# Optimization experiments

Measured on AMD Instinct MI355X. Metric: run time of the kernel, lower is better.

## Reference

```python
import jax, jax.numpy as jnp
import numpy as np

T, B, IN = 1000, 16, 440
H0, H1 = 512, 512


def setup_inputs() -> dict:
    key = jax.random.key(0)
    ks = iter(jax.random.split(key, 64))

    def w(shape, s=0.02):
        return jax.random.normal(next(ks), shape, jnp.float32) * s

    inp = {"x": jax.random.normal(next(ks), (T, B, IN), jnp.float32)}
    # layer 0 consumes IN features; layer 1 consumes 2*H0 (bidir concat)
    for li, (din, h) in enumerate([(IN, H0), (2 * H0, H1)]):
        for g in "fioc":
            inp[f"W{g}{li}"] = w((h, din))          # x-gate Linear weight
            inp[f"b{g}{li}"] = jnp.zeros((h,), jnp.float32)  # x-gate bias
            inp[f"U{g}{li}"] = w((h, h))            # recurrent Linear (no bias)
    return inp


def _lstm_layer(x, Wf, bf, Wi, bi, Wo, bo, Wc, bc, Uf, Ui, Uo, Uc):
    # Precompute input-to-gate projections for all timesteps (as the torch code does).
    gf = jnp.einsum('tbi,hi->tbh', x, Wf) + bf
    gi = jnp.einsum('tbi,hi->tbh', x, Wi) + bi
    go = jnp.einsum('tbi,hi->tbh', x, Wo) + bo
    gc = jnp.einsum('tbi,hi->tbh', x, Wc) + bc
    B2, H = x.shape[1], Wf.shape[0]

    def step(carry, g):
        ht, ct = carry
        gft, git, got, gct = g
        ft = jax.nn.sigmoid(gft + ht @ Uf.T)
        it = jax.nn.sigmoid(git + ht @ Ui.T)
        ot = jax.nn.sigmoid(got + ht @ Uo.T)
        # drop_mask == 1.0 in eval mode (lstm_drop = 0.0)
        ct = it * jnp.tanh(gct + ht @ Uc.T) + ft * ct
        ht = ot * jnp.tanh(ct)
        return (ht, ct), ht

    init = (jnp.zeros((B2, H), x.dtype), jnp.zeros((B2, H), x.dtype))
    _, h = jax.lax.scan(step, init, (gf, gi, go, gc))
    return h  # [T, B2, H]


def _bidir_layer(x, params):
    Bb = x.shape[1]
    # bidir: concat forward stream with time-flipped stream along batch dim
    x2 = jnp.concatenate([x, x[::-1]], axis=1)
    h = _lstm_layer(x2, *params)
    h_f = h[:, :Bb]
    h_b = h[:, Bb:][::-1]  # flip backward stream back to forward time
    return jnp.concatenate([h_f, h_b], axis=2)


def reference(x,
              Wf0, bf0, Uf0, Wi0, bi0, Ui0, Wo0, bo0, Uo0, Wc0, bc0, Uc0,
              Wf1, bf1, Uf1, Wi1, bi1, Ui1, Wo1, bo1, Uo1, Wc1, bc1, Uc1):
    p0 = (Wf0, bf0, Wi0, bi0, Wo0, bo0, Wc0, bc0, Uf0, Ui0, Uo0, Uc0)
    p1 = (Wf1, bf1, Wi1, bi1, Wo1, bo1, Wc1, bc1, Uf1, Ui1, Uo1, Uc1)
    h = _bidir_layer(x, p0)
    h = _bidir_layer(h, p1)
    return h  # [T, B, 2*H1]
```

## Files before the change

### kernel.cpp

```cpp
#include <hip/hip_runtime.h>
#include <hip/hip_bf16.h>
#include <stdint.h>


typedef __attribute__((ext_vector_type(8))) short bf16x8;
typedef __attribute__((ext_vector_type(4))) float f32x4;
typedef __attribute__((ext_vector_type(4))) int i32x4;

__device__ __forceinline__ unsigned short f2bf(float f) {
    union { float f; unsigned int u; } v; v.f = f;
    unsigned int u = v.u;
    return (unsigned short)((u + 0x7fffu + ((u >> 16) & 1u)) >> 16);
}
__device__ __forceinline__ float bf2f(unsigned short b) {
    union { unsigned int u; float f; } v; v.u = ((unsigned int)b) << 16;
    return v.f;
}
__device__ __forceinline__ float fsig(float x) { return 1.f / (1.f + __expf(-x)); }
__device__ __forceinline__ float ftanh(float x) { return 1.f - 2.f / (1.f + __expf(2.f * x)); }


__device__ __forceinline__ unsigned int coh_ld32(const void* p) {
    unsigned int v;
    asm volatile("global_load_dword %0, %1, off sc0 sc1\n\ts_waitcnt vmcnt(0)"
                 : "=v"(v) : "v"(p) : "memory");
    return v;
}
__device__ __forceinline__ void coh_ld128_issue(i32x4& d, const void* p) {
    asm volatile("global_load_dwordx4 %0, %1, off sc0 sc1" : "=&v"(d) : "v"(p) : "memory");
}
__device__ __forceinline__ void coh_st32(void* p, unsigned int v) {
    asm volatile("global_store_dword %0, %1, off sc0 sc1" :: "v"(p), "v"(v) : "memory");
}
__device__ __forceinline__ void vm_drain() {
    asm volatile("s_waitcnt vmcnt(0)" ::: "memory");
}


__global__ void pack_x_kernel(const float* __restrict__ x, unsigned short* __restrict__ xp,
                              int M, int K, int Kp) {
    int total = M * Kp;
    for (int idx = blockIdx.x * blockDim.x + threadIdx.x; idx < total;
         idx += gridDim.x * blockDim.x) {
        int r = idx / Kp, k = idx - r * Kp;
        xp[idx] = (k < K) ? f2bf(x[(size_t)r * K + k]) : (unsigned short)0;
    }
}

__global__ void pack_w_kernel(const float* __restrict__ Wf, const float* __restrict__ Wi,
                              const float* __restrict__ Wo, const float* __restrict__ Wc,
                              unsigned short* __restrict__ out, int K, int Kp) {
    int total = 2048 * Kp;
    for (int idx = blockIdx.x * blockDim.x + threadIdx.x; idx < total;
         idx += gridDim.x * blockDim.x) {
        int n = idx / Kp, k = idx - n * Kp;
        int gate = n >> 9, j = n & 511;
        const float* W = (gate == 0) ? Wf : (gate == 1) ? Wi : (gate == 2) ? Wo : Wc;
        out[idx] = (k < K) ? f2bf(W[(size_t)j * K + k]) : (unsigned short)0;
    }
}


__global__ __launch_bounds__(256) void gemm_gates(
    const unsigned short* __restrict__ A, const unsigned short* __restrict__ Bm,
    const float* __restrict__ bF, const float* __restrict__ bI,
    const float* __restrict__ bO, const float* __restrict__ bC,
    unsigned short* __restrict__ G, int Kp) {
    __shared__ unsigned short Alds[64][32];
    __shared__ unsigned short Blds[64][32];
    const int tid = threadIdx.x;
    const int m0 = blockIdx.x * 64;
    const int n0 = blockIdx.y * 64;
    const int w = tid >> 6, l = tid & 63;
    const int lr = l & 15, lk = (l >> 4) * 8;
    const int ldrow = tid >> 2;
    const int ldk = (tid & 3) * 8;
    const unsigned short* Aptr = A + (size_t)(m0 + ldrow) * Kp + ldk;
    const unsigned short* Bptr = Bm + (size_t)(n0 + ldrow) * Kp + ldk;

    f32x4 zero = {0.f, 0.f, 0.f, 0.f};
    f32x4 acc0 = zero, acc1 = zero, acc2 = zero, acc3 = zero;

    for (int k0 = 0; k0 < Kp; k0 += 32) {
        *(uint4*)&Alds[ldrow][ldk] = *(const uint4*)(Aptr + k0);
        *(uint4*)&Blds[ldrow][ldk] = *(const uint4*)(Bptr + k0);
        __syncthreads();
        bf16x8 a = *(const bf16x8*)&Alds[w * 16 + lr][lk];
        bf16x8 b0 = *(const bf16x8*)&Blds[0 * 16 + lr][lk];
        bf16x8 b1 = *(const bf16x8*)&Blds[1 * 16 + lr][lk];
        bf16x8 b2 = *(const bf16x8*)&Blds[2 * 16 + lr][lk];
        bf16x8 b3 = *(const bf16x8*)&Blds[3 * 16 + lr][lk];
        acc0 = __builtin_amdgcn_mfma_f32_16x16x32_bf16(a, b0, acc0, 0, 0, 0);
        acc1 = __builtin_amdgcn_mfma_f32_16x16x32_bf16(a, b1, acc1, 0, 0, 0);
        acc2 = __builtin_amdgcn_mfma_f32_16x16x32_bf16(a, b2, acc2, 0, 0, 0);
        acc3 = __builtin_amdgcn_mfma_f32_16x16x32_bf16(a, b3, acc3, 0, 0, 0);
        __syncthreads();
    }
    const int gate = n0 >> 9;
    const float* bias = (gate == 0) ? bF : (gate == 1) ? bI : (gate == 2) ? bO : bC;
    f32x4 accs[4] = {acc0, acc1, acc2, acc3};
#pragma unroll
    for (int c = 0; c < 4; ++c) {
        int col = n0 + c * 16 + lr;
        float bv = bias[col & 511];
#pragma unroll
        for (int r = 0; r < 4; ++r) {
            int row = m0 + w * 16 + (l >> 4) * 4 + r;
            G[(size_t)row * 2048 + col] = f2bf(accs[c][r] + bv);
        }
    }
}


template <int LAYER>
__global__ __launch_bounds__(256, 1) void lstm_rec12(
    const unsigned short* __restrict__ U, const unsigned short* __restrict__ G,
    unsigned short* __restrict__ y_bf, float* __restrict__ y_f32,
    unsigned int* __restrict__ h_frag, unsigned int* __restrict__ flags, int T) {
    __shared__ unsigned short wlds[4 * 16 * 64 * 8];
    __shared__ unsigned short hstage[2][16 * 64 * 8 * 2];

    const int tid = threadIdx.x;
    const int w = tid >> 6;
    const int l = tid & 63;
    const int wg = blockIdx.x;
    const int j0 = wg * 16;
    const int g = l & 3;
    const int q = (l & 15) >> 2;
    const int jl = 4 * w + q;
    const int m0 = (l >> 4) * 4 + g;
    const int mrow = (l >> 4) * 4;
    const int colg = g * 512 + j0 + jl;
    const int kcw = wg >> 1;
    const int jlq = ((wg & 1) << 4) + jl;
    const int lslot = m0 + 16 * (jlq >> 3);
    const int jb = jlq & 7;
    const int fid0 = (0 * 16 + kcw) * 256 + lslot * 4 + (jb >> 1);
    const int fid1 = (1 * 16 + kcw) * 256 + lslot * 4 + (jb >> 1);
    unsigned int* const flagp = flags + (size_t)(wg * 4 + w) * 32;
    const unsigned int* const pollp = flags + (size_t)(32 * w + (l & 31)) * 32;

    for (int e = tid; e < 4096; e += 256) {
        int fl = e >> 6;
        int ll = e & 63;
        int nt = fl >> 4, kc = fl & 15;
        int nl = nt * 16 + (ll & 15);
        int jj = nl >> 2, gg = nl & 3;
        int nglob = gg * 512 + j0 + jj;
        int k = kc * 32 + (ll >> 4) * 8;
        *(uint4*)&wlds[(size_t)e * 8] = *(const uint4*)&U[(size_t)nglob * 512 + k];
    }

    unsigned short gpf[2][4];
    {
        const unsigned short* gf_ = G + (size_t)mrow * 2048 + colg;
        const unsigned short* gb_ = G + (size_t)((T - 1) * 16 + mrow) * 2048 + colg;
#pragma unroll
        for (int r = 0; r < 4; ++r) {
            gpf[0][r] = gf_[r * 2048];
            gpf[1][r] = gb_[r * 2048];
        }
    }

    float cst[2][4] = {{0.f, 0.f, 0.f, 0.f}, {0.f, 0.f, 0.f, 0.f}};

    for (int s = 0; s < T; ++s) {
        if (s > 0) {
            {
                const unsigned tgt = (unsigned)(s + 1);
                int guard = 0;
                for (;;) {
                    unsigned u = 0xFFFFFFFFu;
                    if (l < 32) u = coh_ld32(pollp);
                    if (__all(u >= tgt) || ++guard > (1 << 14)) break;
                }
            }
            {
                const unsigned int* src = h_frag + (size_t)(s & 1) * 8192;
                unsigned int* dst = (unsigned int*)hstage[s & 1];
                const int half = (l >> 5);
                i32x4 v[8];
                int gd[8];
#pragma unroll
                for (int i = 0; i < 8; ++i) {
                    int strip = half * 32 + 8 * w + i;
                    gd[i] = strip * 128 + (l & 31) * 4;
                    coh_ld128_issue(v[i], src + gd[i]);
                }
                vm_drain();
                __builtin_amdgcn_sched_barrier(0);
#pragma unroll
                for (int i = 0; i < 8; ++i) *(i32x4*)(dst + gd[i]) = v[i];
            }
        }
        __syncthreads();

        unsigned short gcur[2][4];
#pragma unroll
        for (int r = 0; r < 4; ++r) {
            gcur[0][r] = gpf[0][r];
            gcur[1][r] = gpf[1][r];
        }
        {
            int sn = (s + 1 < T) ? (s + 1) : (T - 1);
            const unsigned short* gf_ = G + (size_t)(sn * 16 + mrow) * 2048 + colg;
            const unsigned short* gb_ = G + (size_t)((T - 1 - sn) * 16 + mrow) * 2048 + colg;
#pragma unroll
            for (int r = 0; r < 4; ++r) {
                gpf[0][r] = gf_[r * 2048];
                gpf[1][r] = gb_[r * 2048];
            }
        }

        f32x4 acc0 = {0.f, 0.f, 0.f, 0.f};
        f32x4 acc1 = {0.f, 0.f, 0.f, 0.f};
        if (s > 0) {
            const unsigned short* hs = hstage[s & 1];
#pragma unroll
            for (int kc = 0; kc < 16; ++kc) {
                bf16x8 a0 = *(const bf16x8*)&hs[((size_t)(0 * 16 + kc) * 64 + l) * 8];
                bf16x8 a1 = *(const bf16x8*)&hs[((size_t)(1 * 16 + kc) * 64 + l) * 8];
                bf16x8 bw = *(const bf16x8*)&wlds[(((size_t)w * 16 + kc) * 64 + l) * 8];
                acc0 = __builtin_amdgcn_mfma_f32_16x16x32_bf16(a0, bw, acc0, 0, 0, 0);
                acc1 = __builtin_amdgcn_mfma_f32_16x16x32_bf16(a1, bw, acc1, 0, 0, 0);
            }
        }

        float hsel[2];
        float hof[2];
        unsigned hww[2];
        unsigned int* hfw = h_frag + (size_t)((s + 1) & 1) * 8192;
#pragma unroll
        for (int mb = 0; mb < 2; ++mb) {
            f32x4 acc = mb ? acc1 : acc0;
            float hn_sel = 0.f;
#pragma unroll
            for (int r = 0; r < 4; ++r) {
                float v = acc[r] + bf2f(gcur[mb][r]);
                float x1 = __shfl_xor(v, 1, 64);
                float x2 = __shfl_xor(v, 2, 64);
                float x3 = __shfl_xor(v, 3, 64);
                bool b0 = (g & 1) != 0, b1 = (g & 2) != 0;
                float gf = b1 ? (b0 ? x3 : x2) : (b0 ? x1 : v);
                float gi = b1 ? (b0 ? x2 : x3) : (b0 ? v : x1);
                float go = b1 ? (b0 ? x1 : v) : (b0 ? x3 : x2);
                float gc = b1 ? (b0 ? v : x1) : (b0 ? x2 : x3);
                float ft = fsig(gf), it = fsig(gi), ot = fsig(go);
                float cn = it * ftanh(gc) + ft * cst[mb][r];
                cst[mb][r] = cn;
                float hn = ot * ftanh(cn);
                if (r == g) hn_sel = hn;
            }
            hsel[mb] = hn_sel;
            unsigned b16 = (unsigned)f2bf(hn_sel);
            unsigned ho = (unsigned)__shfl_xor((int)b16, 4, 64);
            hww[mb] = b16 | (ho << 16);
            hof[mb] = __shfl_xor(hn_sel, 4, 64);
            if ((q & 1) == 0) coh_st32(hfw + (mb ? fid1 : fid0), hww[mb]);
        }

        vm_drain();
        if (l == 0) coh_st32(flagp, (unsigned)(s + 2));

        if ((q & 1) == 0) {
#pragma unroll
            for (int mb = 0; mb < 2; ++mb) {
                int row = (mb ? (T - 1 - s) : s) * 16 + m0;
                int col = mb * 512 + j0 + jl;
                if (LAYER == 0) {
                    *(unsigned int*)&y_bf[(size_t)row * 1024 + col] = hww[mb];
                } else {
                    *(float2*)&y_f32[(size_t)row * 1024 + col] =
                        make_float2(hsel[mb], hof[mb]);
                }
            }
        }
    }
}


extern "C" void kernel_launch(void* const* d_in, const int* in_sizes, int n_in,
                              void* d_out, int out_size, void* d_ws, size_t ws_size,
                              hipStream_t stream) {
    (void)in_sizes; (void)n_in; (void)out_size; (void)ws_size;
    const int T = 1000, M = T * 16;
    const int K0 = 440, K0p = 448, K1 = 1024;

    char* ws = (char*)d_ws;
    size_t off = 0;
    auto alloc = [&](size_t bytes) -> void* {
        void* p = ws + off;
        off += (bytes + 255) & ~(size_t)255;
        return p;
    };
    unsigned short* G  = (unsigned short*)alloc((size_t)M * 2048 * 2);
    unsigned short* xp = (unsigned short*)alloc((size_t)M * K0p * 2);
    unsigned short* W0 = (unsigned short*)alloc((size_t)2048 * K0p * 2);
    unsigned short* W1 = (unsigned short*)alloc((size_t)2048 * K1 * 2);
    unsigned short* U0 = (unsigned short*)alloc((size_t)2048 * 512 * 2);
    unsigned short* U1 = (unsigned short*)alloc((size_t)2048 * 512 * 2);
    unsigned short* y0 = (unsigned short*)alloc((size_t)M * 1024 * 2);
    unsigned int* hf0  = (unsigned int*)alloc((size_t)2 * 8192 * 4);
    unsigned int* hf1  = (unsigned int*)alloc((size_t)2 * 8192 * 4);
    unsigned int* fl0  = (unsigned int*)alloc((size_t)128 * 32 * 4);
    unsigned int* fl1  = (unsigned int*)alloc((size_t)128 * 32 * 4);

    const float* x = (const float*)d_in[0];

    hipMemsetAsync(fl0, 0, 128 * 32 * 4, stream);
    hipMemsetAsync(fl1, 0, 128 * 32 * 4, stream);

    pack_x_kernel<<<2048, 256, 0, stream>>>(x, xp, M, K0, K0p);
    pack_w_kernel<<<1024, 256, 0, stream>>>((const float*)d_in[1], (const float*)d_in[4],
                                            (const float*)d_in[7], (const float*)d_in[10],
                                            W0, K0, K0p);
    pack_w_kernel<<<1024, 256, 0, stream>>>((const float*)d_in[3], (const float*)d_in[6],
                                            (const float*)d_in[9], (const float*)d_in[12],
                                            U0, 512, 512);
    pack_w_kernel<<<1024, 256, 0, stream>>>((const float*)d_in[13], (const float*)d_in[16],
                                            (const float*)d_in[19], (const float*)d_in[22],
                                            W1, K1, K1);
    pack_w_kernel<<<1024, 256, 0, stream>>>((const float*)d_in[15], (const float*)d_in[18],
                                            (const float*)d_in[21], (const float*)d_in[24],
                                            U1, 512, 512);

    dim3 blk(256);
    dim3 g0(M / 64, 2048 / 64);
    gemm_gates<<<g0, blk, 0, stream>>>(xp, W0, (const float*)d_in[2], (const float*)d_in[5],
                                       (const float*)d_in[8], (const float*)d_in[11], G, K0p);
    lstm_rec12<0><<<32, 256, 0, stream>>>(U0, G, y0, nullptr, hf0, fl0, T);
    gemm_gates<<<g0, blk, 0, stream>>>(y0, W1, (const float*)d_in[14], (const float*)d_in[17],
                                       (const float*)d_in[20], (const float*)d_in[23], G, K1);
    lstm_rec12<1><<<32, 256, 0, stream>>>(U1, G, nullptr, (float*)d_out, hf1, fl1, T);
}
```

Measured before the change: 8.850 ms.

## Tag hidden-state exchange words with step number to drop store drain before flag

Each published h value is now written as a 32-bit word carrying the step index in its upper half, and readers validate the tags and re-poll any stale 128-bit chunks. This lets writers post their flag without first draining outstanding stores, moving part of the cross-workgroup handshake into per-word validation. The exchange buffer doubles in size and each step now issues 16 coherent loads per thread instead of 8. The flag poll is still present, so readers wait on both the flag and the tags.

```diff
diff --git a/kernel.cpp b/kernel.cpp
--- a/kernel.cpp
+++ b/kernel.cpp
@@ -113,12 +113,12 @@
 
 
 template <int LAYER>
-__global__ __launch_bounds__(256, 1) void lstm_rec12(
+__global__ __launch_bounds__(256, 1) void lstm_rec13(
     const unsigned short* __restrict__ U, const unsigned short* __restrict__ G,
     unsigned short* __restrict__ y_bf, float* __restrict__ y_f32,
-    unsigned int* __restrict__ h_frag, unsigned int* __restrict__ flags, int T) {
+    unsigned int* __restrict__ tg, unsigned int* __restrict__ flags, int T) {
     __shared__ unsigned short wlds[4 * 16 * 64 * 8];
-    __shared__ unsigned short hstage[2][16 * 64 * 8 * 2];
+    __shared__ unsigned short hstage[2][16384];
 
     const int tid = threadIdx.x;
     const int w = tid >> 6;
@@ -135,8 +135,8 @@
     const int jlq = ((wg & 1) << 4) + jl;
     const int lslot = m0 + 16 * (jlq >> 3);
     const int jb = jlq & 7;
-    const int fid0 = (0 * 16 + kcw) * 256 + lslot * 4 + (jb >> 1);
-    const int fid1 = (1 * 16 + kcw) * 256 + lslot * 4 + (jb >> 1);
+    const int fidx0 = ((0 * 16 + kcw) * 64 + lslot) * 8 + jb;
+    const int fidx1 = ((1 * 16 + kcw) * 64 + lslot) * 8 + jb;
     unsigned int* const flagp = flags + (size_t)(wg * 4 + w) * 32;
     const unsigned int* const pollp = flags + (size_t)(32 * w + (l & 31)) * 32;
 
@@ -176,21 +176,55 @@
                 }
             }
             {
-                const unsigned int* src = h_frag + (size_t)(s & 1) * 8192;
-                unsigned int* dst = (unsigned int*)hstage[s & 1];
-                const int half = (l >> 5);
-                i32x4 v[8];
-                int gd[8];
-#pragma unroll
-                for (int i = 0; i < 8; ++i) {
-                    int strip = half * 32 + 8 * w + i;
-                    gd[i] = strip * 128 + (l & 31) * 4;
-                    coh_ld128_issue(v[i], src + gd[i]);
-                }
+                const uint4* tg4 = (const uint4*)(tg + (size_t)(s & 1) * 16384);
+                const unsigned tagw = (unsigned)s << 16;
+                uint2* dst = (uint2*)hstage[s & 1];
+                i32x4 pend[16];
+                bool okc[16];
+#pragma unroll
+                for (int i = 0; i < 16; ++i)
+                    coh_ld128_issue(pend[i], tg4 + (tid + 256 * i));
                 vm_drain();
                 __builtin_amdgcn_sched_barrier(0);
 #pragma unroll
-                for (int i = 0; i < 8; ++i) *(i32x4*)(dst + gd[i]) = v[i];
+                for (int i = 0; i < 16; ++i) {
+                    unsigned a = (unsigned)pend[i][0], b = (unsigned)pend[i][1];
+                    unsigned c = (unsigned)pend[i][2], d = (unsigned)pend[i][3];
+                    okc[i] = ((a & 0xffff0000u) == tagw) & ((b & 0xffff0000u) == tagw) &
+                             ((c & 0xffff0000u) == tagw) & ((d & 0xffff0000u) == tagw);
+                    uint2 pk;
+                    pk.x = (a & 0xffffu) | (b << 16);
+                    pk.y = (c & 0xffffu) | (d << 16);
+                    dst[tid + 256 * i] = pk;
+                }
+                int rounds = 0;
+                for (;;) {
+                    bool allok = okc[0] & okc[1] & okc[2] & okc[3] & okc[4] & okc[5] &
+                                 okc[6] & okc[7] & okc[8] & okc[9] & okc[10] & okc[11] &
+                                 okc[12] & okc[13] & okc[14] & okc[15];
+                    if (__all((int)allok)) break;
+                    if (++rounds > 1024) break;
+#pragma unroll
+                    for (int i = 0; i < 16; ++i)
+                        if (!okc[i]) coh_ld128_issue(pend[i], tg4 + (tid + 256 * i));
+                    vm_drain();
+                    __builtin_amdgcn_sched_barrier(0);
+#pragma unroll
+                    for (int i = 0; i < 16; ++i) {
+                        if (!okc[i]) {
+                            unsigned a = (unsigned)pend[i][0], b = (unsigned)pend[i][1];
+                            unsigned c = (unsigned)pend[i][2], d = (unsigned)pend[i][3];
+                            okc[i] = ((a & 0xffff0000u) == tagw) &
+                                     ((b & 0xffff0000u) == tagw) &
+                                     ((c & 0xffff0000u) == tagw) &
+                                     ((d & 0xffff0000u) == tagw);
+                            uint2 pk;
+                            pk.x = (a & 0xffffu) | (b << 16);
+                            pk.y = (c & 0xffffu) | (d << 16);
+                            dst[tid + 256 * i] = pk;
+                        }
+                    }
+                }
             }
         }
         __syncthreads();
@@ -226,10 +260,9 @@
             }
         }
 
+        unsigned int* tgw = tg + (size_t)((s + 1) & 1) * 16384;
+        const unsigned tagn = (unsigned)(s + 1) << 16;
         float hsel[2];
-        float hof[2];
-        unsigned hww[2];
-        unsigned int* hfw = h_frag + (size_t)((s + 1) & 1) * 8192;
 #pragma unroll
         for (int mb = 0; mb < 2; ++mb) {
             f32x4 acc = mb ? acc1 : acc0;
@@ -252,26 +285,31 @@
                 if (r == g) hn_sel = hn;
             }
             hsel[mb] = hn_sel;
-            unsigned b16 = (unsigned)f2bf(hn_sel);
+            coh_st32(&tgw[mb ? fidx1 : fidx0], tagn | (unsigned)f2bf(hn_sel));
+        }
+
+        if (l == 0) coh_st32(flagp, (unsigned)(s + 2));
+
+        {
+            unsigned b16 = (unsigned)f2bf(hsel[0]);
             unsigned ho = (unsigned)__shfl_xor((int)b16, 4, 64);
-            hww[mb] = b16 | (ho << 16);
-            hof[mb] = __shfl_xor(hn_sel, 4, 64);
-            if ((q & 1) == 0) coh_st32(hfw + (mb ? fid1 : fid0), hww[mb]);
-        }
-
-        vm_drain();
-        if (l == 0) coh_st32(flagp, (unsigned)(s + 2));
-
-        if ((q & 1) == 0) {
-#pragma unroll
-            for (int mb = 0; mb < 2; ++mb) {
-                int row = (mb ? (T - 1 - s) : s) * 16 + m0;
-                int col = mb * 512 + j0 + jl;
-                if (LAYER == 0) {
-                    *(unsigned int*)&y_bf[(size_t)row * 1024 + col] = hww[mb];
-                } else {
-                    *(float2*)&y_f32[(size_t)row * 1024 + col] =
-                        make_float2(hsel[mb], hof[mb]);
+            unsigned hw0 = b16 | (ho << 16);
+            float ho0 = __shfl_xor(hsel[0], 4, 64);
+            b16 = (unsigned)f2bf(hsel[1]);
+            ho = (unsigned)__shfl_xor((int)b16, 4, 64);
+            unsigned hw1 = b16 | (ho << 16);
+            float ho1 = __shfl_xor(hsel[1], 4, 64);
+            if ((q & 1) == 0) {
+#pragma unroll
+                for (int mb = 0; mb < 2; ++mb) {
+                    int row = (mb ? (T - 1 - s) : s) * 16 + m0;
+                    int col = mb * 512 + j0 + jl;
+                    if (LAYER == 0) {
+                        *(unsigned int*)&y_bf[(size_t)row * 1024 + col] = mb ? hw1 : hw0;
+                    } else {
+                        *(float2*)&y_f32[(size_t)row * 1024 + col] =
+                            make_float2(hsel[mb], mb ? ho1 : ho0);
+                    }
                 }
             }
         }
@@ -300,13 +338,15 @@
     unsigned short* U0 = (unsigned short*)alloc((size_t)2048 * 512 * 2);
     unsigned short* U1 = (unsigned short*)alloc((size_t)2048 * 512 * 2);
     unsigned short* y0 = (unsigned short*)alloc((size_t)M * 1024 * 2);
-    unsigned int* hf0  = (unsigned int*)alloc((size_t)2 * 8192 * 4);
-    unsigned int* hf1  = (unsigned int*)alloc((size_t)2 * 8192 * 4);
+    unsigned int* tg0  = (unsigned int*)alloc((size_t)2 * 16384 * 4);
+    unsigned int* tg1  = (unsigned int*)alloc((size_t)2 * 16384 * 4);
     unsigned int* fl0  = (unsigned int*)alloc((size_t)128 * 32 * 4);
     unsigned int* fl1  = (unsigned int*)alloc((size_t)128 * 32 * 4);
 
     const float* x = (const float*)d_in[0];
 
+    hipMemsetAsync(tg0, 0, (size_t)2 * 16384 * 4, stream);
+    hipMemsetAsync(tg1, 0, (size_t)2 * 16384 * 4, stream);
     hipMemsetAsync(fl0, 0, 128 * 32 * 4, stream);
     hipMemsetAsync(fl1, 0, 128 * 32 * 4, stream);
 
@@ -328,8 +368,8 @@
     dim3 g0(M / 64, 2048 / 64);
     gemm_gates<<<g0, blk, 0, stream>>>(xp, W0, (const float*)d_in[2], (const float*)d_in[5],
                                        (const float*)d_in[8], (const float*)d_in[11], G, K0p);
-    lstm_rec12<0><<<32, 256, 0, stream>>>(U0, G, y0, nullptr, hf0, fl0, T);
+    lstm_rec13<0><<<32, 256, 0, stream>>>(U0, G, y0, nullptr, tg0, fl0, T);
     gemm_gates<<<g0, blk, 0, stream>>>(y0, W1, (const float*)d_in[14], (const float*)d_in[17],
                                        (const float*)d_in[20], (const float*)d_in[23], G, K1);
-    lstm_rec12<1><<<32, 256, 0, stream>>>(U1, G, nullptr, (float*)d_out, hf1, fl1, T);
-}
+    lstm_rec13<1><<<32, 256, 0, stream>>>(U1, G, nullptr, (float*)d_out, tg1, fl1, T);
+}
```

New measurement: 9.655 ms. +9.1%, slower.
